# Performance work log

Hardware: AMD Instinct MI355X
Metric: run time of the kernel (lower is better)

## Reference

```python
import jax, jax.numpy as jnp
import numpy as np

D = 256      # model_dim
H = 8        # num_heads
S = 256      # tokens per channel
CH = [4, 2, 6, 4]  # multiplex_channels_per_sample


def _make_padding(ch, s):
    # Build gather indices / mask mapping packed tokens [T] -> padded [B, Lmax]
    B = len(ch)
    lens = [c * s for c in ch]
    T = sum(lens)
    Lmax = max(lens)
    pad_idx = np.zeros((B, Lmax), dtype=np.int32)
    pad_mask = np.zeros((B, Lmax), dtype=bool)
    off = 0
    for b, L in enumerate(lens):
        pad_idx[b, :L] = np.arange(off, off + L, dtype=np.int32)
        pad_mask[b, :L] = True
        off += L
    return jnp.asarray(pad_idx), jnp.asarray(pad_mask)


def setup_inputs() -> dict:
    key = jax.random.key(0)
    ks = jax.random.split(key, 16)
    C = sum(CH)
    x_query = jax.random.normal(ks[0], (C, S, D), jnp.float32)
    x_keyval = jax.random.normal(ks[1], (C, S, D), jnp.float32)
    pos = jax.random.normal(ks[2], (C, S, D), jnp.float32)
    pad_idx, pad_mask = _make_padding(CH, S)
    sc = 1.0 / np.sqrt(D)
    Wq = jax.random.normal(ks[3], (D, D), jnp.float32) * sc
    Wk = jax.random.normal(ks[4], (D, D), jnp.float32) * sc
    Wv = jax.random.normal(ks[5], (D, D), jnp.float32) * sc
    Wo = jax.random.normal(ks[6], (D, D), jnp.float32) * sc
    bq = jax.random.normal(ks[7], (D,), jnp.float32) * 0.02
    bk = jax.random.normal(ks[8], (D,), jnp.float32) * 0.02
    bv = jax.random.normal(ks[9], (D,), jnp.float32) * 0.02
    bo = jax.random.normal(ks[10], (D,), jnp.float32) * 0.02
    return {"x_query": x_query, "x_keyval": x_keyval, "pos": pos,
            "pad_idx": pad_idx, "pad_mask": pad_mask,
            "Wq": Wq, "bq": bq, "Wk": Wk, "bk": bk,
            "Wv": Wv, "bv": bv, "Wo": Wo, "bo": bo}


def reference(x_query, x_keyval, pos, pad_idx, pad_mask,
              Wq, bq, Wk, bk, Wv, bv, Wo, bo):
    C, s, d = x_query.shape
    T = C * s
    dh = d // H
    # MHA with positional embedding: pos is added to query and key inputs
    # (query_pos = key_pos = pos in the original forward), value is raw.
    q_in = (x_query + pos).reshape(T, d)
    k_in = (x_keyval + pos).reshape(T, d)
    v_in = x_keyval.reshape(T, d)
    q = q_in @ Wq + bq
    k = k_in @ Wk + bk
    v = v_in @ Wv + bv
    # Pad packed ragged tokens into [B, Lmax, D] per cu_seq_len segments
    B, Lmax = pad_idx.shape
    qp = q[pad_idx].reshape(B, Lmax, H, dh)
    kp = k[pad_idx].reshape(B, Lmax, H, dh)
    vp = v[pad_idx].reshape(B, Lmax, H, dh)
    scores = jnp.einsum('bqhd,bkhd->bhqk', qp, kp) / jnp.sqrt(jnp.asarray(dh, q.dtype))
    neg = jnp.asarray(jnp.finfo(scores.dtype).min, scores.dtype)
    scores = jnp.where(pad_mask[:, None, None, :], scores, neg)
    attn = jax.nn.softmax(scores, axis=-1)
    out = jnp.einsum('bhqk,bkhd->bqhd', attn, vp).reshape(B, Lmax, d)
    out = out * pad_mask[..., None]
    # Scatter padded outputs back to packed layout [T, D]
    flat = jnp.zeros((T, d), out.dtype).at[pad_idx.reshape(-1)].add(out.reshape(-1, d))
    flat = flat @ Wo + bo
    return flat.reshape(C, s, d)
```

## Files before the change

kernel.cpp:

```cpp
#include <hip/hip_runtime.h>
#include <math.h>

#define Dm 256
#define Tt 4096

typedef short  s16x8 __attribute__((ext_vector_type(8)));
typedef float  f32x4 __attribute__((ext_vector_type(4)));

__device__ __forceinline__ ushort f2bf(float x) {
    union { float f; unsigned u; } v; v.f = x;
    unsigned r = v.u + 0x7fffu + ((v.u >> 16) & 1u);
    return (ushort)(r >> 16);
}

__global__ __launch_bounds__(256)
void prep_w(const float* __restrict__ Wq, const float* __restrict__ Wk,
            const float* __restrict__ Wv, const float* __restrict__ Wo,
            ushort* __restrict__ Wt)
{
    __shared__ float T[64][65];
    const int tid = threadIdx.x;
    const int m = blockIdx.y;
    const int i = blockIdx.x >> 2, j = blockIdx.x & 3;
    const float* W = (m == 0) ? Wq : (m == 1) ? Wk : (m == 2) ? Wv : Wo;

    #pragma unroll
    for (int s = 0; s < 4; ++s) {
        int idx = s * 256 + tid;
        int r = idx >> 4, c4 = (idx & 15) << 2;
        float4 f = *(const float4*)&W[(i * 64 + r) * Dm + j * 64 + c4];
        T[c4 + 0][r] = f.x; T[c4 + 1][r] = f.y;
        T[c4 + 2][r] = f.z; T[c4 + 3][r] = f.w;
    }
    __syncthreads();
    #pragma unroll
    for (int s = 0; s < 2; ++s) {
        int idx = s * 256 + tid;
        int cr = idx >> 3, k8 = (idx & 7) << 3;
        s16x8 v8;
        #pragma unroll
        for (int jj = 0; jj < 8; ++jj) v8[jj] = (short)f2bf(T[cr][k8 + jj]);
        *(s16x8*)&Wt[m * 65536 + (j * 64 + cr) * Dm + i * 64 + k8] = v8;
    }
}

__global__ __launch_bounds__(256)
void qkv_mfma(const float* __restrict__ xq, const float* __restrict__ xkv,
              const float* __restrict__ pos, const ushort* __restrict__ Wt,
              const float* __restrict__ bq, const float* __restrict__ bk,
              const float* __restrict__ bv,
              ushort* __restrict__ qo, ushort* __restrict__ ko, ushort* __restrict__ vo)
{
    __shared__ __align__(16) ushort A_s[64 * 64];
    __shared__ __align__(16) ushort B_s[64 * 64];
    const int tid = threadIdx.x;
    const int lane = tid & 63, g = lane >> 4, myrow = lane & 15, w = tid >> 6;
    const int t0 = blockIdx.x * 64;
    const int c0 = blockIdx.y * 64;
    const int m  = blockIdx.z;
    const float*  xin  = (m == 0) ? xq : xkv;
    const ushort* WT   = Wt + m * 65536;
    const float*  bias = (m == 0) ? bq : (m == 1) ? bk : bv;
    ushort*       out  = (m == 0) ? qo : (m == 1) ? ko : vo;

    f32x4 acc[4] = {};
    for (int ks = 0; ks < 4; ++ks) {
        const int k0 = ks * 64;
        #pragma unroll
        for (int s = 0; s < 2; ++s) {
            int idx = s * 256 + tid;
            int r = idx >> 3, c = idx & 7;
            const float* p0 = &xin[(t0 + r) * Dm + k0 + c * 8];
            float4 fa = *(const float4*)p0;
            float4 fb = *(const float4*)(p0 + 4);
            if (m < 2) {
                const float* pp = &pos[(t0 + r) * Dm + k0 + c * 8];
                float4 pa = *(const float4*)pp, pb = *(const float4*)(pp + 4);
                fa.x += pa.x; fa.y += pa.y; fa.z += pa.z; fa.w += pa.w;
                fb.x += pb.x; fb.y += pb.y; fb.z += pb.z; fb.w += pb.w;
            }
            s16x8 v8;
            v8[0] = (short)f2bf(fa.x); v8[1] = (short)f2bf(fa.y);
            v8[2] = (short)f2bf(fa.z); v8[3] = (short)f2bf(fa.w);
            v8[4] = (short)f2bf(fb.x); v8[5] = (short)f2bf(fb.y);
            v8[6] = (short)f2bf(fb.z); v8[7] = (short)f2bf(fb.w);
            *(s16x8*)&A_s[r * 64 + ((c ^ (r & 7)) << 3)] = v8;
            *(s16x8*)&B_s[r * 64 + ((c ^ (r & 7)) << 3)] =
                *(const s16x8*)&WT[(c0 + r) * Dm + k0 + c * 8];
        }
        __syncthreads();
        const int arow = w * 16 + myrow;
        #pragma unroll
        for (int kk = 0; kk < 2; ++kk) {
            s16x8 a = *(s16x8*)&A_s[arow * 64 + (((g + 4 * kk) ^ (arow & 7)) << 3)];
            #pragma unroll
            for (int ct = 0; ct < 4; ++ct) {
                int brow = ct * 16 + myrow;
                s16x8 b = *(s16x8*)&B_s[brow * 64 + (((g + 4 * kk) ^ (brow & 7)) << 3)];
                acc[ct] = __builtin_amdgcn_mfma_f32_16x16x32_bf16(a, b, acc[ct], 0, 0, 0);
            }
        }
        __syncthreads();
    }
    const float qsc = 0.17677669529663687f;
    #pragma unroll
    for (int ct = 0; ct < 4; ++ct) {
        float bval = bias[c0 + ct * 16 + myrow];
        #pragma unroll
        for (int r = 0; r < 4; ++r) {
            float vv = acc[ct][r] + bval;
            if (m == 0) vv *= qsc;
            out[(t0 + w * 16 + 4 * g + r) * Dm + c0 + ct * 16 + myrow] = f2bf(vv);
        }
    }
}

__global__ __launch_bounds__(256)
void attn_mfma(const ushort* __restrict__ q, const ushort* __restrict__ k,
               const ushort* __restrict__ v, ushort* __restrict__ o)
{
    __shared__ __align__(16) ushort K_s[64 * 32];
    __shared__ __align__(16) ushort V_s[32 * 64];
    __shared__ __align__(16) ushort P_s[4][16 * 64];
    const int tid = threadIdx.x;
    const int lane = tid & 63, g = lane >> 4, myrow = lane & 15, w = tid >> 6;
    const int h = blockIdx.x & 7, chunk = blockIdx.x >> 3;

    int cstart, off, L;
    if (chunk < 16)      { cstart = 0;  off = 0;    L = 1024; }
    else if (chunk < 24) { cstart = 16; off = 1024; L = 512;  }
    else if (chunk < 48) { cstart = 24; off = 1536; L = 1536; }
    else                 { cstart = 48; off = 3072; L = 1024; }
    const int qrow0 = off + (chunk - cstart) * 64;

    const s16x8 qf = *(const s16x8*)&q[(qrow0 + w * 16 + myrow) * Dm + h * 32 + g * 8];

    f32x4 accO0 = {}, accO1 = {};
    float mrun[4] = {-INFINITY, -INFINITY, -INFINITY, -INFINITY};
    float lrun[4] = {};

    for (int kb = 0; kb < L; kb += 64) {
        if (tid < 128) {
            #pragma unroll
            for (int s = 0; s < 2; ++s) {
                int idx = s * 128 + tid;
                int row = idx >> 2, c8 = (idx & 3) << 3;
                *(s16x8*)&K_s[row * 32 + c8] =
                    *(const s16x8*)&k[(off + kb + row) * Dm + h * 32 + c8];
            }
        } else {
            int t = tid - 128;
            #pragma unroll
            for (int s = 0; s < 2; ++s) {
                int idx = s * 128 + t;
                int key = idx >> 2, c8 = (idx & 3) << 3;
                s16x8 vv = *(const s16x8*)&v[(off + kb + key) * Dm + h * 32 + c8];
                #pragma unroll
                for (int i = 0; i < 8; ++i) {
                    int dh = c8 + i;
                    V_s[dh * 64 + (((key >> 3) ^ (dh & 7)) << 3) + (key & 7)] = (ushort)vv[i];
                }
            }
        }
        __syncthreads();

        const f32x4 zero = {};
        f32x4 s4[4];
        #pragma unroll
        for (int kt = 0; kt < 4; ++kt) {
            s16x8 bk = *(s16x8*)&K_s[(kt * 16 + myrow) * 32 + g * 8];
            s4[kt] = __builtin_amdgcn_mfma_f32_16x16x32_bf16(qf, bk, zero, 0, 0, 0);
        }
        float mt[4], scale[4], psum[4];
        #pragma unroll
        for (int r = 0; r < 4; ++r) {
            float a = fmaxf(fmaxf(s4[0][r], s4[1][r]), fmaxf(s4[2][r], s4[3][r]));
            a = fmaxf(a, __shfl_xor(a, 1));
            a = fmaxf(a, __shfl_xor(a, 2));
            a = fmaxf(a, __shfl_xor(a, 4));
            a = fmaxf(a, __shfl_xor(a, 8));
            mt[r] = a;
        }
        #pragma unroll
        for (int r = 0; r < 4; ++r) {
            float mn = fmaxf(mrun[r], mt[r]);
            scale[r] = __expf(mrun[r] - mn);
            mrun[r] = mn;
            psum[r] = 0.f;
        }
        #pragma unroll
        for (int kt = 0; kt < 4; ++kt) {
            #pragma unroll
            for (int r = 0; r < 4; ++r) {
                float p = __expf(s4[kt][r] - mrun[r]);
                psum[r] += p;
                int qq = 4 * g + r;
                int key = myrow + 16 * kt;
                P_s[w][qq * 64 + (((key >> 3) ^ (qq & 7)) << 3) + (key & 7)] = f2bf(p);
            }
        }
        #pragma unroll
        for (int r = 0; r < 4; ++r) {
            float sps = psum[r];
            sps += __shfl_xor(sps, 1);
            sps += __shfl_xor(sps, 2);
            sps += __shfl_xor(sps, 4);
            sps += __shfl_xor(sps, 8);
            lrun[r] = lrun[r] * scale[r] + sps;
            accO0[r] *= scale[r];
            accO1[r] *= scale[r];
        }
        asm volatile("s_waitcnt lgkmcnt(0)" ::: "memory");
        #pragma unroll
        for (int kk = 0; kk < 2; ++kk) {
            s16x8 ap = *(s16x8*)&P_s[w][myrow * 64 + (((g + 4 * kk) ^ (myrow & 7)) << 3)];
            s16x8 b0 = *(s16x8*)&V_s[myrow * 64 + (((4 * kk + g) ^ (myrow & 7)) << 3)];
            s16x8 b1 = *(s16x8*)&V_s[(16 + myrow) * 64 + (((4 * kk + g) ^ (myrow & 7)) << 3)];
            accO0 = __builtin_amdgcn_mfma_f32_16x16x32_bf16(ap, b0, accO0, 0, 0, 0);
            accO1 = __builtin_amdgcn_mfma_f32_16x16x32_bf16(ap, b1, accO1, 0, 0, 0);
        }
        __syncthreads();
    }
    #pragma unroll
    for (int r = 0; r < 4; ++r) {
        float inv = 1.0f / lrun[r];
        int row = (qrow0 + w * 16 + 4 * g + r) * Dm + h * 32;
        o[row + myrow]      = f2bf(accO0[r] * inv);
        o[row + 16 + myrow] = f2bf(accO1[r] * inv);
    }
}

__global__ __launch_bounds__(256)
void oproj_mfma(const ushort* __restrict__ A, const ushort* __restrict__ Wt3,
                const float* __restrict__ bo, float* __restrict__ out)
{
    __shared__ __align__(16) ushort A_s[64 * 64];
    __shared__ __align__(16) ushort B_s[64 * 64];
    const int tid = threadIdx.x;
    const int lane = tid & 63, g = lane >> 4, myrow = lane & 15, w = tid >> 6;
    const int t0 = blockIdx.x * 64;
    const int c0 = blockIdx.y * 64;

    f32x4 acc[4] = {};
    for (int ks = 0; ks < 4; ++ks) {
        const int k0 = ks * 64;
        #pragma unroll
        for (int s = 0; s < 2; ++s) {
            int idx = s * 256 + tid;
            int r = idx >> 3, c = idx & 7;
            *(s16x8*)&A_s[r * 64 + ((c ^ (r & 7)) << 3)] =
                *(const s16x8*)&A[(t0 + r) * Dm + k0 + c * 8];
            *(s16x8*)&B_s[r * 64 + ((c ^ (r & 7)) << 3)] =
                *(const s16x8*)&Wt3[(c0 + r) * Dm + k0 + c * 8];
        }
        __syncthreads();
        const int arow = w * 16 + myrow;
        #pragma unroll
        for (int kk = 0; kk < 2; ++kk) {
            s16x8 a = *(s16x8*)&A_s[arow * 64 + (((g + 4 * kk) ^ (arow & 7)) << 3)];
            #pragma unroll
            for (int ct = 0; ct < 4; ++ct) {
                int brow = ct * 16 + myrow;
                s16x8 b = *(s16x8*)&B_s[brow * 64 + (((g + 4 * kk) ^ (brow & 7)) << 3)];
                acc[ct] = __builtin_amdgcn_mfma_f32_16x16x32_bf16(a, b, acc[ct], 0, 0, 0);
            }
        }
        __syncthreads();
    }
    #pragma unroll
    for (int ct = 0; ct < 4; ++ct) {
        float bval = bo[c0 + ct * 16 + myrow];
        #pragma unroll
        for (int r = 0; r < 4; ++r)
            out[(t0 + w * 16 + 4 * g + r) * Dm + c0 + ct * 16 + myrow] = acc[ct][r] + bval;
    }
}

extern "C" void kernel_launch(void* const* d_in, const int* in_sizes, int n_in,
                              void* d_out, int out_size, void* d_ws, size_t ws_size,
                              hipStream_t stream) {
    const float* xq  = (const float*)d_in[0];
    const float* xkv = (const float*)d_in[1];
    const float* pos = (const float*)d_in[2];
    const float* Wq  = (const float*)d_in[5];
    const float* bq  = (const float*)d_in[6];
    const float* Wk  = (const float*)d_in[7];
    const float* bk  = (const float*)d_in[8];
    const float* Wv  = (const float*)d_in[9];
    const float* bv  = (const float*)d_in[10];
    const float* Wo  = (const float*)d_in[11];
    const float* bo  = (const float*)d_in[12];

    ushort* qb = (ushort*)d_ws;
    ushort* kb = qb + Tt * Dm;
    ushort* vb = kb + Tt * Dm;
    ushort* ab = vb + Tt * Dm;
    ushort* Wt = ab + Tt * Dm;

    prep_w<<<dim3(16, 4), 256, 0, stream>>>(Wq, Wk, Wv, Wo, Wt);
    qkv_mfma<<<dim3(64, 4, 3), 256, 0, stream>>>(xq, xkv, pos, Wt, bq, bk, bv,
                                                 qb, kb, vb);
    attn_mfma<<<dim3(512), 256, 0, stream>>>(qb, kb, vb, ab);
    oproj_mfma<<<dim3(64, 4), 256, 0, stream>>>(ab, Wt + 3 * 65536, bo, (float*)d_out);
}
```

Before: 138.5 us.

## Split attention keys across waves, pre-convert inputs, transpose V, shrink oproj tiles

Input conversion (x+pos to bf16) becomes its own kernel, so the projection GEMM reads bf16 tiles instead of converting floats once for each of the four column blocks. V is written transposed so attention can load it with vector loads, with no per-element shuffle into shared memory. Attention now uses 32-query tiles with each wave handling a quarter of the keys, giving twice as many blocks. Each wave uses register-prefetched, wave-private LDS buffers with no block barriers, and the waves' partial softmax states are merged at the end. The output projection uses 32-token tiles to double the grid, at the cost of an extra launch and extra workspace traffic.

Result: no change. 140.5 us (+1.5%).

```diff
diff --git a/kernel.cpp b/kernel.cpp
--- a/kernel.cpp
+++ b/kernel.cpp
@@ -11,6 +11,41 @@
     union { float f; unsigned u; } v; v.f = x;
     unsigned r = v.u + 0x7fffu + ((v.u >> 16) & 1u);
     return (ushort)(r >> 16);
+}
+
+__device__ __forceinline__ int ppos(int row, int key) {
+    return row * 64 + (key & 7) + ((((key >> 3) ^ (row >> 1)) & 7) << 3);
+}
+
+__global__ __launch_bounds__(256)
+void convert_x(const float* __restrict__ xq, const float* __restrict__ xkv,
+               const float* __restrict__ pos,
+               ushort* __restrict__ A0, ushort* __restrict__ A1, ushort* __restrict__ A2)
+{
+    const int t = threadIdx.x;
+    const int m = blockIdx.y;
+    const float* xin = (m == 0) ? xq : xkv;
+    ushort* out = (m == 0) ? A0 : (m == 1) ? A1 : A2;
+    const int token = blockIdx.x * 32 + (t >> 3);
+    const int c0 = (t & 7) * 32;
+    const float* p = &xin[token * Dm + c0];
+    const float* pp = &pos[token * Dm + c0];
+    #pragma unroll
+    for (int i = 0; i < 4; ++i) {
+        float4 fa = *(const float4*)&p[i * 8];
+        float4 fb = *(const float4*)&p[i * 8 + 4];
+        if (m < 2) {
+            float4 pa = *(const float4*)&pp[i * 8], pb = *(const float4*)&pp[i * 8 + 4];
+            fa.x += pa.x; fa.y += pa.y; fa.z += pa.z; fa.w += pa.w;
+            fb.x += pb.x; fb.y += pb.y; fb.z += pb.z; fb.w += pb.w;
+        }
+        s16x8 v8;
+        v8[0] = (short)f2bf(fa.x); v8[1] = (short)f2bf(fa.y);
+        v8[2] = (short)f2bf(fa.z); v8[3] = (short)f2bf(fa.w);
+        v8[4] = (short)f2bf(fb.x); v8[5] = (short)f2bf(fb.y);
+        v8[6] = (short)f2bf(fb.z); v8[7] = (short)f2bf(fb.w);
+        *(s16x8*)&out[token * Dm + c0 + i * 8] = v8;
+    }
 }
 
 __global__ __launch_bounds__(256)
@@ -45,11 +80,11 @@
 }
 
 __global__ __launch_bounds__(256)
-void qkv_mfma(const float* __restrict__ xq, const float* __restrict__ xkv,
-              const float* __restrict__ pos, const ushort* __restrict__ Wt,
-              const float* __restrict__ bq, const float* __restrict__ bk,
-              const float* __restrict__ bv,
-              ushort* __restrict__ qo, ushort* __restrict__ ko, ushort* __restrict__ vo)
+void proj_gemm(const ushort* __restrict__ A0, const ushort* __restrict__ A1,
+               const ushort* __restrict__ A2, const ushort* __restrict__ Wt,
+               const float* __restrict__ bq, const float* __restrict__ bk,
+               const float* __restrict__ bv,
+               ushort* __restrict__ qo, ushort* __restrict__ ko, ushort* __restrict__ vT)
 {
     __shared__ __align__(16) ushort A_s[64 * 64];
     __shared__ __align__(16) ushort B_s[64 * 64];
@@ -58,10 +93,9 @@
     const int t0 = blockIdx.x * 64;
     const int c0 = blockIdx.y * 64;
     const int m  = blockIdx.z;
-    const float*  xin  = (m == 0) ? xq : xkv;
-    const ushort* WT   = Wt + m * 65536;
-    const float*  bias = (m == 0) ? bq : (m == 1) ? bk : bv;
-    ushort*       out  = (m == 0) ? qo : (m == 1) ? ko : vo;
+    const ushort* Ab = (m == 0) ? A0 : (m == 1) ? A1 : A2;
+    const ushort* WT = Wt + m * 65536;
+    const float* bias = (m == 0) ? bq : (m == 1) ? bk : bv;
 
     f32x4 acc[4] = {};
     for (int ks = 0; ks < 4; ++ks) {
@@ -70,21 +104,8 @@
         for (int s = 0; s < 2; ++s) {
             int idx = s * 256 + tid;
             int r = idx >> 3, c = idx & 7;
-            const float* p0 = &xin[(t0 + r) * Dm + k0 + c * 8];
-            float4 fa = *(const float4*)p0;
-            float4 fb = *(const float4*)(p0 + 4);
-            if (m < 2) {
-                const float* pp = &pos[(t0 + r) * Dm + k0 + c * 8];
-                float4 pa = *(const float4*)pp, pb = *(const float4*)(pp + 4);
-                fa.x += pa.x; fa.y += pa.y; fa.z += pa.z; fa.w += pa.w;
-                fb.x += pb.x; fb.y += pb.y; fb.z += pb.z; fb.w += pb.w;
-            }
-            s16x8 v8;
-            v8[0] = (short)f2bf(fa.x); v8[1] = (short)f2bf(fa.y);
-            v8[2] = (short)f2bf(fa.z); v8[3] = (short)f2bf(fa.w);
-            v8[4] = (short)f2bf(fb.x); v8[5] = (short)f2bf(fb.y);
-            v8[6] = (short)f2bf(fb.z); v8[7] = (short)f2bf(fb.w);
-            *(s16x8*)&A_s[r * 64 + ((c ^ (r & 7)) << 3)] = v8;
+            *(s16x8*)&A_s[r * 64 + ((c ^ (r & 7)) << 3)] =
+                *(const s16x8*)&Ab[(t0 + r) * Dm + k0 + c * 8];
             *(s16x8*)&B_s[r * 64 + ((c ^ (r & 7)) << 3)] =
                 *(const s16x8*)&WT[(c0 + r) * Dm + k0 + c * 8];
         }
@@ -105,128 +126,175 @@
     const float qsc = 0.17677669529663687f;
     #pragma unroll
     for (int ct = 0; ct < 4; ++ct) {
-        float bval = bias[c0 + ct * 16 + myrow];
+        int col = c0 + ct * 16 + myrow;
+        float bval = bias[col];
         #pragma unroll
         for (int r = 0; r < 4; ++r) {
+            int tok = t0 + w * 16 + 4 * g + r;
             float vv = acc[ct][r] + bval;
-            if (m == 0) vv *= qsc;
-            out[(t0 + w * 16 + 4 * g + r) * Dm + c0 + ct * 16 + myrow] = f2bf(vv);
-        }
-    }
-}
-
-__global__ __launch_bounds__(256)
-void attn_mfma(const ushort* __restrict__ q, const ushort* __restrict__ k,
-               const ushort* __restrict__ v, ushort* __restrict__ o)
-{
-    __shared__ __align__(16) ushort K_s[64 * 32];
-    __shared__ __align__(16) ushort V_s[32 * 64];
+            if (m == 0)      qo[tok * Dm + col] = f2bf(vv * qsc);
+            else if (m == 1) ko[tok * Dm + col] = f2bf(vv);
+            else             vT[col * Tt + tok] = f2bf(vv);
+        }
+    }
+}
+
+__global__ __launch_bounds__(256)
+void attn2(const ushort* __restrict__ q, const ushort* __restrict__ kb,
+           const ushort* __restrict__ vT, ushort* __restrict__ o)
+{
+    __shared__ __align__(16) ushort K_s[4][64 * 32];
+    __shared__ __align__(16) ushort V_s[4][32 * 64];
     __shared__ __align__(16) ushort P_s[4][16 * 64];
     const int tid = threadIdx.x;
     const int lane = tid & 63, g = lane >> 4, myrow = lane & 15, w = tid >> 6;
-    const int h = blockIdx.x & 7, chunk = blockIdx.x >> 3;
-
-    int cstart, off, L;
-    if (chunk < 16)      { cstart = 0;  off = 0;    L = 1024; }
-    else if (chunk < 24) { cstart = 16; off = 1024; L = 512;  }
-    else if (chunk < 48) { cstart = 24; off = 1536; L = 1536; }
-    else                 { cstart = 48; off = 3072; L = 1024; }
-    const int qrow0 = off + (chunk - cstart) * 64;
-
-    const s16x8 qf = *(const s16x8*)&q[(qrow0 + w * 16 + myrow) * Dm + h * 32 + g * 8];
-
-    f32x4 accO0 = {}, accO1 = {};
-    float mrun[4] = {-INFINITY, -INFINITY, -INFINITY, -INFINITY};
-    float lrun[4] = {};
-
-    for (int kb = 0; kb < L; kb += 64) {
-        if (tid < 128) {
-            #pragma unroll
-            for (int s = 0; s < 2; ++s) {
-                int idx = s * 128 + tid;
-                int row = idx >> 2, c8 = (idx & 3) << 3;
-                *(s16x8*)&K_s[row * 32 + c8] =
-                    *(const s16x8*)&k[(off + kb + row) * Dm + h * 32 + c8];
-            }
-        } else {
-            int t = tid - 128;
-            #pragma unroll
-            for (int s = 0; s < 2; ++s) {
-                int idx = s * 128 + t;
-                int key = idx >> 2, c8 = (idx & 3) << 3;
-                s16x8 vv = *(const s16x8*)&v[(off + kb + key) * Dm + h * 32 + c8];
+    const int h = blockIdx.x & 7, qt = blockIdx.x >> 3;
+
+    int off, L;
+    if (qt < 32)      { off = 0;    L = 1024; }
+    else if (qt < 48) { off = 1024; L = 512;  }
+    else if (qt < 96) { off = 1536; L = 1536; }
+    else              { off = 3072; L = 1024; }
+    const int qrow0 = qt * 32;
+    const int Lw = L >> 2;
+    const int kbeg = off + w * Lw;
+    const int nt = Lw >> 6;
+
+    s16x8 qf[2];
+    qf[0] = *(const s16x8*)&q[(qrow0 + myrow) * Dm + h * 32 + g * 8];
+    qf[1] = *(const s16x8*)&q[(qrow0 + 16 + myrow) * Dm + h * 32 + g * 8];
+
+    f32x4 aO[2][2] = {};
+    float mr[2][4], lr[2][4];
+    #pragma unroll
+    for (int s = 0; s < 2; ++s)
+        #pragma unroll
+        for (int r = 0; r < 4; ++r) { mr[s][r] = -INFINITY; lr[s][r] = 0.f; }
+
+    s16x8 kr[4], vr[4];
+    #define LOAD_TILE(kc) do {                                                          \
+        int kcc = (kc);                                                                 \
+        _Pragma("unroll")                                                               \
+        for (int i = 0; i < 4; ++i) {                                                   \
+            int idx = i * 64 + lane;                                                    \
+            kr[i] = *(const s16x8*)&kb[(kcc + (idx >> 2)) * Dm + h * 32 + ((idx & 3) << 3)]; \
+            vr[i] = *(const s16x8*)&vT[(h * 32 + (lane >> 3) + i * 8) * Tt + kcc + ((lane & 7) << 3)]; \
+        }                                                                               \
+    } while (0)
+
+    LOAD_TILE(kbeg);
+    for (int t = 0; t < nt; ++t) {
+        asm volatile("s_waitcnt vmcnt(0) lgkmcnt(0)" ::: "memory");
+        __builtin_amdgcn_sched_barrier(0);
+        #pragma unroll
+        for (int i = 0; i < 4; ++i) {
+            int idx = i * 64 + lane;
+            *(s16x8*)&K_s[w][(idx >> 2) * 32 + ((idx & 3) << 3)] = kr[i];
+            int dh = (lane >> 3) + i * 8;
+            *(s16x8*)&V_s[w][dh * 64 + (((lane & 7) ^ (dh & 7)) << 3)] = vr[i];
+        }
+        if (t + 1 < nt) LOAD_TILE(kbeg + (t + 1) * 64);
+        asm volatile("s_waitcnt lgkmcnt(0)" ::: "memory");
+        __builtin_amdgcn_sched_barrier(0);
+
+        #pragma unroll
+        for (int s = 0; s < 2; ++s) {
+            const f32x4 zero = {};
+            f32x4 s4[4];
+            #pragma unroll
+            for (int kt = 0; kt < 4; ++kt) {
+                s16x8 bkf = *(const s16x8*)&K_s[w][(kt * 16 + myrow) * 32 + g * 8];
+                s4[kt] = __builtin_amdgcn_mfma_f32_16x16x32_bf16(qf[s], bkf, zero, 0, 0, 0);
+            }
+            float mt[4], sc[4], ps[4];
+            #pragma unroll
+            for (int r = 0; r < 4; ++r) {
+                float a = fmaxf(fmaxf(s4[0][r], s4[1][r]), fmaxf(s4[2][r], s4[3][r]));
+                a = fmaxf(a, __shfl_xor(a, 1));
+                a = fmaxf(a, __shfl_xor(a, 2));
+                a = fmaxf(a, __shfl_xor(a, 4));
+                a = fmaxf(a, __shfl_xor(a, 8));
+                mt[r] = a;
+            }
+            #pragma unroll
+            for (int r = 0; r < 4; ++r) {
+                float mn = fmaxf(mr[s][r], mt[r]);
+                sc[r] = __expf(mr[s][r] - mn);
+                mr[s][r] = mn;
+                ps[r] = 0.f;
+            }
+            asm volatile("s_waitcnt lgkmcnt(0)" ::: "memory");
+            __builtin_amdgcn_sched_barrier(0);
+            #pragma unroll
+            for (int kt = 0; kt < 4; ++kt) {
                 #pragma unroll
-                for (int i = 0; i < 8; ++i) {
-                    int dh = c8 + i;
-                    V_s[dh * 64 + (((key >> 3) ^ (dh & 7)) << 3) + (key & 7)] = (ushort)vv[i];
+                for (int r = 0; r < 4; ++r) {
+                    float p = __expf(s4[kt][r] - mr[s][r]);
+                    ps[r] += p;
+                    P_s[w][ppos(4 * g + r, 16 * kt + myrow)] = f2bf(p);
                 }
             }
-        }
-        __syncthreads();
-
-        const f32x4 zero = {};
-        f32x4 s4[4];
-        #pragma unroll
-        for (int kt = 0; kt < 4; ++kt) {
-            s16x8 bk = *(s16x8*)&K_s[(kt * 16 + myrow) * 32 + g * 8];
-            s4[kt] = __builtin_amdgcn_mfma_f32_16x16x32_bf16(qf, bk, zero, 0, 0, 0);
-        }
-        float mt[4], scale[4], psum[4];
-        #pragma unroll
-        for (int r = 0; r < 4; ++r) {
-            float a = fmaxf(fmaxf(s4[0][r], s4[1][r]), fmaxf(s4[2][r], s4[3][r]));
-            a = fmaxf(a, __shfl_xor(a, 1));
-            a = fmaxf(a, __shfl_xor(a, 2));
-            a = fmaxf(a, __shfl_xor(a, 4));
-            a = fmaxf(a, __shfl_xor(a, 8));
-            mt[r] = a;
-        }
-        #pragma unroll
-        for (int r = 0; r < 4; ++r) {
-            float mn = fmaxf(mrun[r], mt[r]);
-            scale[r] = __expf(mrun[r] - mn);
-            mrun[r] = mn;
-            psum[r] = 0.f;
-        }
-        #pragma unroll
-        for (int kt = 0; kt < 4; ++kt) {
-            #pragma unroll
-            for (int r = 0; r < 4; ++r) {
-                float p = __expf(s4[kt][r] - mrun[r]);
-                psum[r] += p;
-                int qq = 4 * g + r;
-                int key = myrow + 16 * kt;
-                P_s[w][qq * 64 + (((key >> 3) ^ (qq & 7)) << 3) + (key & 7)] = f2bf(p);
-            }
-        }
-        #pragma unroll
-        for (int r = 0; r < 4; ++r) {
-            float sps = psum[r];
-            sps += __shfl_xor(sps, 1);
-            sps += __shfl_xor(sps, 2);
-            sps += __shfl_xor(sps, 4);
-            sps += __shfl_xor(sps, 8);
-            lrun[r] = lrun[r] * scale[r] + sps;
-            accO0[r] *= scale[r];
-            accO1[r] *= scale[r];
-        }
-        asm volatile("s_waitcnt lgkmcnt(0)" ::: "memory");
-        #pragma unroll
-        for (int kk = 0; kk < 2; ++kk) {
-            s16x8 ap = *(s16x8*)&P_s[w][myrow * 64 + (((g + 4 * kk) ^ (myrow & 7)) << 3)];
-            s16x8 b0 = *(s16x8*)&V_s[myrow * 64 + (((4 * kk + g) ^ (myrow & 7)) << 3)];
-            s16x8 b1 = *(s16x8*)&V_s[(16 + myrow) * 64 + (((4 * kk + g) ^ (myrow & 7)) << 3)];
-            accO0 = __builtin_amdgcn_mfma_f32_16x16x32_bf16(ap, b0, accO0, 0, 0, 0);
-            accO1 = __builtin_amdgcn_mfma_f32_16x16x32_bf16(ap, b1, accO1, 0, 0, 0);
-        }
-        __syncthreads();
-    }
-    #pragma unroll
-    for (int r = 0; r < 4; ++r) {
-        float inv = 1.0f / lrun[r];
-        int row = (qrow0 + w * 16 + 4 * g + r) * Dm + h * 32;
-        o[row + myrow]      = f2bf(accO0[r] * inv);
-        o[row + 16 + myrow] = f2bf(accO1[r] * inv);
+            #pragma unroll
+            for (int r = 0; r < 4; ++r) {
+                float sps = ps[r];
+                sps += __shfl_xor(sps, 1);
+                sps += __shfl_xor(sps, 2);
+                sps += __shfl_xor(sps, 4);
+                sps += __shfl_xor(sps, 8);
+                lr[s][r] = lr[s][r] * sc[r] + sps;
+                aO[s][0][r] *= sc[r];
+                aO[s][1][r] *= sc[r];
+            }
+            asm volatile("s_waitcnt lgkmcnt(0)" ::: "memory");
+            __builtin_amdgcn_sched_barrier(0);
+            #pragma unroll
+            for (int kk = 0; kk < 2; ++kk) {
+                s16x8 ap = *(const s16x8*)&P_s[w][ppos(myrow, (g + 4 * kk) * 8)];
+                s16x8 b0 = *(const s16x8*)&V_s[w][myrow * 64 + (((4 * kk + g) ^ (myrow & 7)) << 3)];
+                s16x8 b1 = *(const s16x8*)&V_s[w][(16 + myrow) * 64 + (((4 * kk + g) ^ (myrow & 7)) << 3)];
+                aO[s][0] = __builtin_amdgcn_mfma_f32_16x16x32_bf16(ap, b0, aO[s][0], 0, 0, 0);
+                aO[s][1] = __builtin_amdgcn_mfma_f32_16x16x32_bf16(ap, b1, aO[s][1], 0, 0, 0);
+            }
+        }
+    }
+    #undef LOAD_TILE
+
+    __syncthreads();
+    float* cmb = (float*)&K_s[0][0];
+    if (w > 0) {
+        #pragma unroll
+        for (int s = 0; s < 2; ++s)
+            #pragma unroll
+            for (int r = 0; r < 4; ++r) {
+                int row = (w - 1) * 32 + s * 16 + 4 * g + r;
+                cmb[row * 36 + myrow]      = aO[s][0][r];
+                cmb[row * 36 + 16 + myrow] = aO[s][1][r];
+                if (myrow == 0) { cmb[row * 36 + 32] = mr[s][r]; cmb[row * 36 + 33] = lr[s][r]; }
+            }
+    }
+    __syncthreads();
+    if (w == 0) {
+        #pragma unroll
+        for (int s = 0; s < 2; ++s) {
+            #pragma unroll
+            for (int r = 0; r < 4; ++r) {
+                #pragma unroll
+                for (int ww = 0; ww < 3; ++ww) {
+                    int row = ww * 32 + s * 16 + 4 * g + r;
+                    float m2 = cmb[row * 36 + 32], l2 = cmb[row * 36 + 33];
+                    float mn = fmaxf(mr[s][r], m2);
+                    float a1 = __expf(mr[s][r] - mn), a2 = __expf(m2 - mn);
+                    mr[s][r] = mn;
+                    lr[s][r] = lr[s][r] * a1 + l2 * a2;
+                    aO[s][0][r] = aO[s][0][r] * a1 + cmb[row * 36 + myrow] * a2;
+                    aO[s][1][r] = aO[s][1][r] * a1 + cmb[row * 36 + 16 + myrow] * a2;
+                }
+                float inv = 1.0f / lr[s][r];
+                int orow = (qrow0 + s * 16 + 4 * g + r) * Dm + h * 32;
+                o[orow + myrow]      = f2bf(aO[s][0][r] * inv);
+                o[orow + 16 + myrow] = f2bf(aO[s][1][r] * inv);
+            }
+        }
     }
 }
 
@@ -234,33 +302,37 @@
 void oproj_mfma(const ushort* __restrict__ A, const ushort* __restrict__ Wt3,
                 const float* __restrict__ bo, float* __restrict__ out)
 {
-    __shared__ __align__(16) ushort A_s[64 * 64];
+    __shared__ __align__(16) ushort A_s[32 * 64];
     __shared__ __align__(16) ushort B_s[64 * 64];
     const int tid = threadIdx.x;
     const int lane = tid & 63, g = lane >> 4, myrow = lane & 15, w = tid >> 6;
-    const int t0 = blockIdx.x * 64;
+    const int sh = w >> 1, ch = w & 1;
+    const int t0 = blockIdx.x * 32;
     const int c0 = blockIdx.y * 64;
 
-    f32x4 acc[4] = {};
+    f32x4 acc[2] = {};
     for (int ks = 0; ks < 4; ++ks) {
         const int k0 = ks * 64;
+        {
+            int r = tid >> 3, c = tid & 7;
+            *(s16x8*)&A_s[r * 64 + ((c ^ (r & 7)) << 3)] =
+                *(const s16x8*)&A[(t0 + r) * Dm + k0 + c * 8];
+        }
         #pragma unroll
         for (int s = 0; s < 2; ++s) {
             int idx = s * 256 + tid;
             int r = idx >> 3, c = idx & 7;
-            *(s16x8*)&A_s[r * 64 + ((c ^ (r & 7)) << 3)] =
-                *(const s16x8*)&A[(t0 + r) * Dm + k0 + c * 8];
             *(s16x8*)&B_s[r * 64 + ((c ^ (r & 7)) << 3)] =
                 *(const s16x8*)&Wt3[(c0 + r) * Dm + k0 + c * 8];
         }
         __syncthreads();
-        const int arow = w * 16 + myrow;
+        const int arow = sh * 16 + myrow;
         #pragma unroll
         for (int kk = 0; kk < 2; ++kk) {
             s16x8 a = *(s16x8*)&A_s[arow * 64 + (((g + 4 * kk) ^ (arow & 7)) << 3)];
             #pragma unroll
-            for (int ct = 0; ct < 4; ++ct) {
-                int brow = ct * 16 + myrow;
+            for (int ct = 0; ct < 2; ++ct) {
+                int brow = ch * 32 + ct * 16 + myrow;
                 s16x8 b = *(s16x8*)&B_s[brow * 64 + (((g + 4 * kk) ^ (brow & 7)) << 3)];
                 acc[ct] = __builtin_amdgcn_mfma_f32_16x16x32_bf16(a, b, acc[ct], 0, 0, 0);
             }
@@ -268,11 +340,12 @@
         __syncthreads();
     }
     #pragma unroll
-    for (int ct = 0; ct < 4; ++ct) {
-        float bval = bo[c0 + ct * 16 + myrow];
+    for (int ct = 0; ct < 2; ++ct) {
+        int col = c0 + ch * 32 + ct * 16 + myrow;
+        float bval = bo[col];
         #pragma unroll
         for (int r = 0; r < 4; ++r)
-            out[(t0 + w * 16 + 4 * g + r) * Dm + c0 + ct * 16 + myrow] = acc[ct][r] + bval;
+            out[(t0 + sh * 16 + 4 * g + r) * Dm + col] = acc[ct][r] + bval;
     }
 }
 
@@ -291,15 +364,18 @@
     const float* Wo  = (const float*)d_in[11];
     const float* bo  = (const float*)d_in[12];
 
-    ushort* qb = (ushort*)d_ws;
-    ushort* kb = qb + Tt * Dm;
-    ushort* vb = kb + Tt * Dm;
-    ushort* ab = vb + Tt * Dm;
-    ushort* Wt = ab + Tt * Dm;
-
+    ushort* Abf = (ushort*)d_ws;
+    ushort* qb  = Abf + 3 * Tt * Dm;
+    ushort* kbp = qb + Tt * Dm;
+    ushort* vT  = kbp + Tt * Dm;
+    ushort* ab  = vT + Tt * Dm;
+    ushort* Wt  = ab + Tt * Dm;
+
+    convert_x<<<dim3(Tt / 32, 3), 256, 0, stream>>>(xq, xkv, pos, Abf,
+                                                    Abf + Tt * Dm, Abf + 2 * Tt * Dm);
     prep_w<<<dim3(16, 4), 256, 0, stream>>>(Wq, Wk, Wv, Wo, Wt);
-    qkv_mfma<<<dim3(64, 4, 3), 256, 0, stream>>>(xq, xkv, pos, Wt, bq, bk, bv,
-                                                 qb, kb, vb);
-    attn_mfma<<<dim3(512), 256, 0, stream>>>(qb, kb, vb, ab);
-    oproj_mfma<<<dim3(64, 4), 256, 0, stream>>>(ab, Wt + 3 * 65536, bo, (float*)d_out);
-}
+    proj_gemm<<<dim3(64, 4, 3), 256, 0, stream>>>(Abf, Abf + Tt * Dm, Abf + 2 * Tt * Dm,
+                                                  Wt, bq, bk, bv, qb, kbp, vT);
+    attn2<<<dim3(1024), 256, 0, stream>>>(qb, kbp, vT, ab);
+    oproj_mfma<<<dim3(128, 4), 256, 0, stream>>>(ab, Wt + 3 * 65536, bo, (float*)d_out);
+}
```
